# Performance work log

Measured on AMD Instinct MI355X. Metric: run time of the kernel, lower is better.

The kernel has to match this reference:

```python
import jax, jax.numpy as jnp
import numpy as np

N_NODES = 50000
N_EDGES = 800000
IN_FEAT = 256
DIM_H = 64
DIM_OUT = 64


def setup_inputs() -> dict:
    key = jax.random.key(0)
    ks = jax.random.split(key, 9)
    x = jax.random.normal(ks[0], (N_NODES, IN_FEAT), dtype=jnp.float32)
    edge_index = jax.random.randint(ks[1], (2, N_EDGES), 0, N_NODES, dtype=jnp.int64)
    s_in = 1.0 / np.sqrt(IN_FEAT)
    s_h = 1.0 / np.sqrt(DIM_H)
    W_src = jax.random.normal(ks[2], (IN_FEAT, DIM_H), dtype=jnp.float32) * s_in
    W_dst = jax.random.normal(ks[3], (IN_FEAT, DIM_H), dtype=jnp.float32) * s_in
    att_src = jax.random.normal(ks[4], (DIM_H,), dtype=jnp.float32) * s_h
    att_dst = jax.random.normal(ks[5], (DIM_H,), dtype=jnp.float32) * s_h
    bias_conv = jax.random.normal(ks[6], (DIM_H,), dtype=jnp.float32) * 0.01
    W_lin = jax.random.normal(ks[7], (DIM_H, DIM_OUT), dtype=jnp.float32) * s_h
    b_lin = jax.random.normal(ks[8], (DIM_OUT,), dtype=jnp.float32) * 0.01
    return {"x": x, "edge_index": edge_index, "W_src": W_src, "W_dst": W_dst,
            "att_src": att_src, "att_dst": att_dst, "bias_conv": bias_conv,
            "W_lin": W_lin, "b_lin": b_lin}


def reference(x, edge_index, W_src, W_dst, att_src, att_dst, bias_conv, W_lin, b_lin):
    N = x.shape[0]
    src, dst = edge_index[0], edge_index[1]
    # linear projections (GATConv lin_src / lin_dst, no bias)
    h_src = x @ W_src                      # [N, H]
    h_dst = x @ W_dst                      # [N, H]
    # per-node attention logits
    a_src = h_src @ att_src                # [N]
    a_dst = h_dst @ att_dst                # [N]
    # edge-wise score: leaky_relu(a_src[src] + a_dst[dst])
    e = jax.nn.leaky_relu(a_src[src] + a_dst[dst], negative_slope=0.2)  # [E]
    # segment softmax over destination neighborhoods
    e_max = jax.ops.segment_max(e, dst, num_segments=N)
    e_exp = jnp.exp(e - e_max[dst])
    denom = jax.ops.segment_sum(e_exp, dst, num_segments=N)
    alpha = e_exp / denom[dst]             # [E]
    # weighted scatter-add aggregation
    msg = h_src[src] * alpha[:, None]      # [E, H]
    out = jax.ops.segment_sum(msg, dst, num_segments=N) + bias_conv  # [N, H]
    h = jax.nn.relu(out)
    return h @ W_lin + b_lin               # [N, dim_out]
```

## Files before the change

### kernel.cpp

```cpp
#include <hip/hip_runtime.h>
#include <math.h>

#define N_NODES 50000
#define N_EDGES 800000
#define IN_FEAT 256
#define DIM_H   64
#define NPAD    50176
#define CAP     48
#define NBUK    392
#define BNODES  128
#define BCAP    3072
#define EPB     4096
#define PBLKS   784
#define ABLKS   196
#define SPLIT   4
#define PNODES  32

typedef __attribute__((ext_vector_type(8)))  short  s16x8;
typedef __attribute__((ext_vector_type(16))) float  f32x16;

__device__ __forceinline__ float bcast_f(float v, int k) {
  return __int_as_float(__builtin_amdgcn_readlane(__float_as_int(v), k));
}
__device__ __forceinline__ short f2bf(float f) {
  unsigned u = __float_as_uint(f);
  u += 0x7fffu + ((u >> 16) & 1u);
  return (short)(u >> 16);
}

__global__ __launch_bounds__(256, 4) void proj_binA_kernel(
    const float* __restrict__ x,
    const float* __restrict__ Wsrc,
    const float* __restrict__ Wdst,
    const float* __restrict__ att_src,
    const float* __restrict__ att_dst,
    const int* __restrict__ ei,
    unsigned* __restrict__ hbf,
    float* __restrict__ a_src,
    float* __restrict__ a_dst,
    int* __restrict__ gbc,
    unsigned* __restrict__ binbuf) {
  __shared__ short wfrag[16 * 2 * 64 * 8];
  __shared__ float wdl[IN_FEAT];
  __shared__ float attl[DIM_H];

  const int tid = threadIdx.x;

  if (blockIdx.x >= PBLKS) {
    int* bcnt = (int*)wfrag;
    int* wcur = bcnt + NBUK;
    const int e0 = (blockIdx.x - PBLKS) * EPB;

    for (int b = tid; b < NBUK; b += 256) bcnt[b] = 0;
    __syncthreads();

    int dst[16];
    #pragma unroll
    for (int i = 0; i < 16; ++i) {
      int e = e0 + tid + 256 * i;
      dst[i] = (e < N_EDGES) ? ei[N_EDGES + e] : -1;
      if (dst[i] >= 0) atomicAdd(&bcnt[dst[i] >> 7], 1);
    }
    __syncthreads();

    for (int b = tid; b < NBUK; b += 256) {
      int c = bcnt[b];
      wcur[b] = c ? atomicAdd(&gbc[b], c) : 0;
    }
    __syncthreads();

    #pragma unroll
    for (int i = 0; i < 16; ++i) {
      int e = e0 + tid + 256 * i;
      if (e < N_EDGES) {
        int s = ei[e];
        int b = dst[i] >> 7;
        int pos = atomicAdd(&wcur[b], 1);
        if (pos < BCAP)
          binbuf[(long)b * BCAP + pos] =
              (unsigned)s | ((unsigned)(dst[i] & 127) << 16);
      }
    }
    return;
  }

  const int lane = tid & 63;
  const int wv   = tid >> 6;
  const int tile = wv >> 1;
  const int h    = wv & 1;

  if (tid < DIM_H) attl[tid] = att_dst[tid];
  __syncthreads();

  {
    float s = 0.f;
    const float4* row = (const float4*)(Wdst + (long)tid * DIM_H);
    #pragma unroll
    for (int q = 0; q < 16; ++q) {
      float4 r = row[q];
      s = fmaf(r.x, attl[4 * q + 0], s);
      s = fmaf(r.y, attl[4 * q + 1], s);
      s = fmaf(r.z, attl[4 * q + 2], s);
      s = fmaf(r.w, attl[4 * q + 3], s);
    }
    wdl[tid] = s;
  }

  for (int e = tid; e < IN_FEAT * DIM_H; e += 256) {
    int k = e >> 6, n = e & 63;
    int s = k >> 4, half = (k >> 3) & 1, j = k & 7, t = n >> 5;
    int fl = (n & 31) + 32 * half;
    wfrag[((s * 2 + t) * 64 + fl) * 8 + j] = f2bf(Wsrc[e]);
  }
  __syncthreads();

  const int base  = blockIdx.x * 64 + tile * 32;
  int row = base + (lane & 31); if (row > N_NODES - 1) row = N_NODES - 1;
  const int koff8 = (lane >> 5) * 8;
  const int k0    = h * 128;
  const float* px = x + (long)row * IN_FEAT + k0 + koff8;

  f32x16 acc0, acc1;
  #pragma unroll
  for (int i = 0; i < 16; ++i) { acc0[i] = 0.f; acc1[i] = 0.f; }
  float pd = 0.f;

  #pragma unroll
  for (int s = 0; s < 8; ++s) {
    float4 va = *(const float4*)(px + s * 16);
    float4 vb = *(const float4*)(px + s * 16 + 4);
    const float* wp = wdl + k0 + s * 16 + koff8;
    float4 w1 = *(const float4*)(wp);
    float4 w2 = *(const float4*)(wp + 4);
    pd = fmaf(va.x, w1.x, pd); pd = fmaf(va.y, w1.y, pd);
    pd = fmaf(va.z, w1.z, pd); pd = fmaf(va.w, w1.w, pd);
    pd = fmaf(vb.x, w2.x, pd); pd = fmaf(vb.y, w2.y, pd);
    pd = fmaf(vb.z, w2.z, pd); pd = fmaf(vb.w, w2.w, pd);
    s16x8 a;
    a[0] = f2bf(va.x); a[1] = f2bf(va.y); a[2] = f2bf(va.z); a[3] = f2bf(va.w);
    a[4] = f2bf(vb.x); a[5] = f2bf(vb.y); a[6] = f2bf(vb.z); a[7] = f2bf(vb.w);
    const int f = (h * 8 + s) * 2;
    s16x8 b0 = *(const s16x8*)(wfrag + ((f + 0) * 64 + lane) * 8);
    s16x8 b1 = *(const s16x8*)(wfrag + ((f + 1) * 64 + lane) * 8);
    acc0 = __builtin_amdgcn_mfma_f32_32x32x16_bf16(a, b0, acc0, 0, 0, 0);
    acc1 = __builtin_amdgcn_mfma_f32_32x32x16_bf16(a, b1, acc1, 0, 0, 0);
  }
  float pds = pd + __shfl_xor(pd, 32, 64);

  __syncthreads();
  float* fa = (float*)wfrag;
  float* myslot = fa + tile * 2304 + lane * 36;
  float* pdb    = fa + 4608 + tile * 32;

  if (h == 1) {
    #pragma unroll
    for (int i = 0; i < 4; ++i)
      *(float4*)(myslot + i * 4) =
          make_float4(acc0[4 * i], acc0[4 * i + 1], acc0[4 * i + 2], acc0[4 * i + 3]);
    #pragma unroll
    for (int i = 0; i < 4; ++i)
      *(float4*)(myslot + 16 + i * 4) =
          make_float4(acc1[4 * i], acc1[4 * i + 1], acc1[4 * i + 2], acc1[4 * i + 3]);
    if (lane < 32) pdb[lane] = pds;
  }
  __syncthreads();
  if (h == 1) return;

  #pragma unroll
  for (int i = 0; i < 4; ++i) {
    float4 t = *(const float4*)(myslot + i * 4);
    acc0[4 * i] += t.x; acc0[4 * i + 1] += t.y;
    acc0[4 * i + 2] += t.z; acc0[4 * i + 3] += t.w;
  }
  #pragma unroll
  for (int i = 0; i < 4; ++i) {
    float4 t = *(const float4*)(myslot + 16 + i * 4);
    acc1[4 * i] += t.x; acc1[4 * i + 1] += t.y;
    acc1[4 * i + 2] += t.z; acc1[4 * i + 3] += t.w;
  }
  pds += pdb[lane & 31];

  const int col = lane & 31;
  const int rhi = 4 * (lane >> 5);

  #pragma unroll
  for (int r = 0; r < 16; ++r) {
    int node = base + (r & 3) + 8 * (r >> 2) + rhi;
    if (node < N_NODES) {
      unsigned p = (unsigned)(unsigned short)f2bf(acc0[r]) |
                   ((unsigned)(unsigned short)f2bf(acc1[r]) << 16);
      hbf[(long)node * 32 + col] = p;
    }
  }

  float att0 = att_src[col];
  float att1 = att_src[col + 32];
  #pragma unroll
  for (int r = 0; r < 16; ++r) {
    float t = acc0[r] * att0 + acc1[r] * att1;
    t += __shfl_xor(t, 1, 64);
    t += __shfl_xor(t, 2, 64);
    t += __shfl_xor(t, 4, 64);
    t += __shfl_xor(t, 8, 64);
    t += __shfl_xor(t, 16, 64);
    int node = base + (r & 3) + 8 * (r >> 2) + rhi;
    if (col == 0 && node < N_NODES) a_src[node] = t;
  }

  int node = base + (lane & 31);
  if (lane < 32 && node < N_NODES) a_dst[node] = pds;
}

__global__ __launch_bounds__(256) void gatherfused_kernel(
    const unsigned* __restrict__ binbuf,
    const int* __restrict__ gbc,
    const float* __restrict__ a_src,
    const float* __restrict__ a_dst,
    const unsigned* __restrict__ hbf,
    const float* __restrict__ bias_conv,
    const float* __restrict__ W_lin,
    const float* __restrict__ b_lin,
    float* __restrict__ out) {
  __shared__ unsigned rec[PNODES * CAP];
  __shared__ int   lcnt[PNODES];
  __shared__ float adl[PNODES];
  __shared__ float wl[64 * 64];

  const int tid    = threadIdx.x;
  const int bucket = blockIdx.x >> 2;
  const int part   = blockIdx.x & 3;
  const int nb     = bucket * BNODES + part * PNODES;
  const int dlo    = part * PNODES;

  {
    const float4* wsrc4 = (const float4*)W_lin;
    float4* wl4 = (float4*)wl;
    for (int i = tid; i < 1024; i += 256) wl4[i] = wsrc4[i];
  }
  if (tid < PNODES) {
    lcnt[tid] = 0;
    adl[tid]  = a_dst[nb + tid];
  }
  __syncthreads();

  int count = gbc[bucket]; if (count > BCAP) count = BCAP;
  const unsigned* bb = binbuf + (long)bucket * BCAP;
  for (int i = tid; i < count; i += 256) {
    unsigned u = bb[i];
    int dl = (int)(u >> 16) - dlo;
    if ((unsigned)dl < PNODES) {
      int s = (int)(u & 0xffffu);
      float sc = a_src[s] + adl[dl];
      sc = sc >= 0.f ? sc : 0.2f * sc;
      float w = __expf(sc);
      int pos = atomicAdd(&lcnt[dl], 1);
      if (pos < CAP)
        rec[dl * CAP + pos] =
            ((unsigned)(unsigned short)f2bf(w) << 16) | (u & 0xffffu);
    }
  }
  __syncthreads();

  const int lane = tid & 63;
  const int wv   = __builtin_amdgcn_readfirstlane(tid >> 6);
  const int grp8 = lane >> 3;
  const int ql8  = lane & 7;
  const float bj  = bias_conv[lane];
  const float blj = b_lin[lane];

  for (int q = 0; q < 8; ++q) {
    const int dl = wv * 8 + q;
    const int n  = nb + dl;
    int m = lcnt[dl]; if (m > CAP) m = CAP;

    float alo[4] = {0.f, 0.f, 0.f, 0.f};
    float ahi[4] = {0.f, 0.f, 0.f, 0.f};
    float den = 0.f;

    for (int j = 0; j < m; j += 16) {
      int idx0 = j + grp8;
      int idx1 = j + 8 + grp8;
      int ci0 = idx0 < m ? idx0 : m - 1;
      int ci1 = idx1 < m ? idx1 : m - 1;
      unsigned u0 = rec[dl * CAP + ci0];
      unsigned u1 = rec[dl * CAP + ci1];
      float w0 = __uint_as_float(u0 & 0xffff0000u);
      float w1 = __uint_as_float(u1 & 0xffff0000u);
      if (idx0 >= m) w0 = 0.f;
      if (idx1 >= m) w1 = 0.f;
      int s0 = (int)(u0 & 0xffffu);
      int s1 = (int)(u1 & 0xffffu);
      uint4 hp0 = *(const uint4*)(hbf + (long)s0 * 32 + ql8 * 4);
      uint4 hp1 = *(const uint4*)(hbf + (long)s1 * 32 + ql8 * 4);
      alo[0] = fmaf(w0, __uint_as_float(hp0.x << 16),         alo[0]);
      ahi[0] = fmaf(w0, __uint_as_float(hp0.x & 0xffff0000u), ahi[0]);
      alo[1] = fmaf(w0, __uint_as_float(hp0.y << 16),         alo[1]);
      ahi[1] = fmaf(w0, __uint_as_float(hp0.y & 0xffff0000u), ahi[1]);
      alo[2] = fmaf(w0, __uint_as_float(hp0.z << 16),         alo[2]);
      ahi[2] = fmaf(w0, __uint_as_float(hp0.z & 0xffff0000u), ahi[2]);
      alo[3] = fmaf(w0, __uint_as_float(hp0.w << 16),         alo[3]);
      ahi[3] = fmaf(w0, __uint_as_float(hp0.w & 0xffff0000u), ahi[3]);
      den += w0;
      alo[0] = fmaf(w1, __uint_as_float(hp1.x << 16),         alo[0]);
      ahi[0] = fmaf(w1, __uint_as_float(hp1.x & 0xffff0000u), ahi[0]);
      alo[1] = fmaf(w1, __uint_as_float(hp1.y << 16),         alo[1]);
      ahi[1] = fmaf(w1, __uint_as_float(hp1.y & 0xffff0000u), ahi[1]);
      alo[2] = fmaf(w1, __uint_as_float(hp1.z << 16),         alo[2]);
      ahi[2] = fmaf(w1, __uint_as_float(hp1.z & 0xffff0000u), ahi[2]);
      alo[3] = fmaf(w1, __uint_as_float(hp1.w << 16),         alo[3]);
      ahi[3] = fmaf(w1, __uint_as_float(hp1.w & 0xffff0000u), ahi[3]);
      den += w1;
    }

    #pragma unroll
    for (int mm = 8; mm <= 32; mm <<= 1) {
      #pragma unroll
      for (int c = 0; c < 4; ++c) {
        alo[c] += __shfl_xor(alo[c], mm, 64);
        ahi[c] += __shfl_xor(ahi[c], mm, 64);
      }
      den += __shfl_xor(den, mm, 64);
    }
    int srcl = (lane & 31) >> 2;
    float v0 = __shfl(alo[0], srcl, 64);
    float v1 = __shfl(alo[1], srcl, 64);
    float v2 = __shfl(alo[2], srcl, 64);
    float v3 = __shfl(alo[3], srcl, 64);
    float v4 = __shfl(ahi[0], srcl, 64);
    float v5 = __shfl(ahi[1], srcl, 64);
    float v6 = __shfl(ahi[2], srcl, 64);
    float v7 = __shfl(ahi[3], srcl, 64);
    int c4 = lane & 3;
    float losel = (c4 == 0) ? v0 : (c4 == 1) ? v1 : (c4 == 2) ? v2 : v3;
    float hisel = (c4 == 0) ? v4 : (c4 == 1) ? v5 : (c4 == 2) ? v6 : v7;
    float accl = (lane >> 5) ? hisel : losel;

    float inv = den > 0.f ? 1.0f / den : 0.f;
    float z = fmaf(accl, inv, bj);
    float h = fmaxf(z, 0.f);
    float o0 = blj, o1 = 0.f, o2 = 0.f, o3 = 0.f;
    #pragma unroll
    for (int k = 0; k < 64; k += 4) {
      o0 = fmaf(bcast_f(h, k + 0), wl[(k + 0) * 64 + lane], o0);
      o1 = fmaf(bcast_f(h, k + 1), wl[(k + 1) * 64 + lane], o1);
      o2 = fmaf(bcast_f(h, k + 2), wl[(k + 2) * 64 + lane], o2);
      o3 = fmaf(bcast_f(h, k + 3), wl[(k + 3) * 64 + lane], o3);
    }
    float o = (o0 + o1) + (o2 + o3);
    if (n < N_NODES) out[(long)n * DIM_H + lane] = o;
  }
}

extern "C" void kernel_launch(void* const* d_in, const int* in_sizes, int n_in,
                              void* d_out, int out_size, void* d_ws, size_t ws_size,
                              hipStream_t stream) {
  const float* x        = (const float*)d_in[0];
  const int*   ei       = (const int*)d_in[1];
  const float* Wsrc     = (const float*)d_in[2];
  const float* Wdst     = (const float*)d_in[3];
  const float* att_src  = (const float*)d_in[4];
  const float* att_dst  = (const float*)d_in[5];
  const float* bias_cv  = (const float*)d_in[6];
  const float* W_lin    = (const float*)d_in[7];
  const float* b_lin    = (const float*)d_in[8];
  float* out = (float*)d_out;

  unsigned* hbf    = (unsigned*)d_ws;
  float*    a_src  = (float*)(hbf + 1600000);
  float*    a_dst  = a_src + NPAD;
  int*      gbc    = (int*)(a_dst + NPAD);
  unsigned* binbuf = (unsigned*)(gbc + 512);

  hipMemsetAsync(gbc, 0, 512 * sizeof(int), stream);

  proj_binA_kernel<<<PBLKS + ABLKS, 256, 0, stream>>>(
      x, Wsrc, Wdst, att_src, att_dst, ei, hbf, a_src, a_dst, gbc, binbuf);

  gatherfused_kernel<<<NBUK * SPLIT, 256, 0, stream>>>(
      binbuf, gbc, a_src, a_dst, hbf, bias_cv, W_lin, b_lin, out);
}
```

Measured before the change: 176.8 us.

## Bin edges into 32-node buckets so each gather block reads only its edges

The edge binning stage now uses 1568 buckets of 32 destination nodes, where it previously used 392 buckets of 128. Before, each of four gather blocks per bucket scanned all 3072 records and discarded three quarters of them; now each gather block reads exactly its own bucket, which removes that redundant global read and filter work. The W_src bf16 fragment fill is also vectorised to load float4 values. The cost is more global bucket-counter atomics and more shared-memory counters in the binning blocks. Per-bucket capacity (768) has less slack, so it could overflow if degree skew were high.

```diff
diff --git a/kernel.cpp b/kernel.cpp
--- a/kernel.cpp
+++ b/kernel.cpp
@@ -7,13 +7,11 @@
 #define DIM_H   64
 #define NPAD    50176
 #define CAP     48
-#define NBUK    392
-#define BNODES  128
-#define BCAP    3072
+#define NBUK2   1568
+#define BCAP2   768
 #define EPB     4096
 #define PBLKS   784
 #define ABLKS   196
-#define SPLIT   4
 #define PNODES  32
 
 typedef __attribute__((ext_vector_type(8)))  short  s16x8;
@@ -48,10 +46,10 @@
 
   if (blockIdx.x >= PBLKS) {
     int* bcnt = (int*)wfrag;
-    int* wcur = bcnt + NBUK;
+    int* wcur = bcnt + NBUK2;
     const int e0 = (blockIdx.x - PBLKS) * EPB;
 
-    for (int b = tid; b < NBUK; b += 256) bcnt[b] = 0;
+    for (int b = tid; b < NBUK2; b += 256) bcnt[b] = 0;
     __syncthreads();
 
     int dst[16];
@@ -59,11 +57,11 @@
     for (int i = 0; i < 16; ++i) {
       int e = e0 + tid + 256 * i;
       dst[i] = (e < N_EDGES) ? ei[N_EDGES + e] : -1;
-      if (dst[i] >= 0) atomicAdd(&bcnt[dst[i] >> 7], 1);
+      if (dst[i] >= 0) atomicAdd(&bcnt[dst[i] >> 5], 1);
     }
     __syncthreads();
 
-    for (int b = tid; b < NBUK; b += 256) {
+    for (int b = tid; b < NBUK2; b += 256) {
       int c = bcnt[b];
       wcur[b] = c ? atomicAdd(&gbc[b], c) : 0;
     }
@@ -74,11 +72,11 @@
       int e = e0 + tid + 256 * i;
       if (e < N_EDGES) {
         int s = ei[e];
-        int b = dst[i] >> 7;
+        int b = dst[i] >> 5;
         int pos = atomicAdd(&wcur[b], 1);
-        if (pos < BCAP)
-          binbuf[(long)b * BCAP + pos] =
-              (unsigned)s | ((unsigned)(dst[i] & 127) << 16);
+        if (pos < BCAP2)
+          binbuf[(long)b * BCAP2 + pos] =
+              (unsigned)s | ((unsigned)(dst[i] & 31) << 16);
       }
     }
     return;
@@ -106,11 +104,15 @@
     wdl[tid] = s;
   }
 
-  for (int e = tid; e < IN_FEAT * DIM_H; e += 256) {
-    int k = e >> 6, n = e & 63;
-    int s = k >> 4, half = (k >> 3) & 1, j = k & 7, t = n >> 5;
-    int fl = (n & 31) + 32 * half;
-    wfrag[((s * 2 + t) * 64 + fl) * 8 + j] = f2bf(Wsrc[e]);
+  for (int e4 = tid * 4; e4 < IN_FEAT * DIM_H; e4 += 1024) {
+    float4 w4 = *(const float4*)(Wsrc + e4);
+    int k = e4 >> 6, n0 = e4 & 63;
+    int s = k >> 4, half = (k >> 3) & 1, j = k & 7, t = n0 >> 5;
+    short* p = &wfrag[((s * 2 + t) * 64 + ((n0 & 31) + 32 * half)) * 8 + j];
+    p[0]  = f2bf(w4.x);
+    p[8]  = f2bf(w4.y);
+    p[16] = f2bf(w4.z);
+    p[24] = f2bf(w4.w);
   }
   __syncthreads();
 
@@ -227,10 +229,8 @@
   __shared__ float wl[64 * 64];
 
   const int tid    = threadIdx.x;
-  const int bucket = blockIdx.x >> 2;
-  const int part   = blockIdx.x & 3;
-  const int nb     = bucket * BNODES + part * PNODES;
-  const int dlo    = part * PNODES;
+  const int bucket = blockIdx.x;
+  const int nb     = bucket * PNODES;
 
   {
     const float4* wsrc4 = (const float4*)W_lin;
@@ -243,21 +243,19 @@
   }
   __syncthreads();
 
-  int count = gbc[bucket]; if (count > BCAP) count = BCAP;
-  const unsigned* bb = binbuf + (long)bucket * BCAP;
+  int count = gbc[bucket]; if (count > BCAP2) count = BCAP2;
+  const unsigned* bb = binbuf + (long)bucket * BCAP2;
   for (int i = tid; i < count; i += 256) {
     unsigned u = bb[i];
-    int dl = (int)(u >> 16) - dlo;
-    if ((unsigned)dl < PNODES) {
-      int s = (int)(u & 0xffffu);
-      float sc = a_src[s] + adl[dl];
-      sc = sc >= 0.f ? sc : 0.2f * sc;
-      float w = __expf(sc);
-      int pos = atomicAdd(&lcnt[dl], 1);
-      if (pos < CAP)
-        rec[dl * CAP + pos] =
-            ((unsigned)(unsigned short)f2bf(w) << 16) | (u & 0xffffu);
-    }
+    int dl = (int)(u >> 16);
+    int s  = (int)(u & 0xffffu);
+    float sc = a_src[s] + adl[dl];
+    sc = sc >= 0.f ? sc : 0.2f * sc;
+    float w = __expf(sc);
+    int pos = atomicAdd(&lcnt[dl], 1);
+    if (pos < CAP)
+      rec[dl * CAP + pos] =
+          ((unsigned)(unsigned short)f2bf(w) << 16) | (u & 0xffffu);
   }
   __syncthreads();
 
@@ -369,13 +367,13 @@
   float*    a_src  = (float*)(hbf + 1600000);
   float*    a_dst  = a_src + NPAD;
   int*      gbc    = (int*)(a_dst + NPAD);
-  unsigned* binbuf = (unsigned*)(gbc + 512);
-
-  hipMemsetAsync(gbc, 0, 512 * sizeof(int), stream);
+  unsigned* binbuf = (unsigned*)(gbc + 2048);
+
+  hipMemsetAsync(gbc, 0, 2048 * sizeof(int), stream);
 
   proj_binA_kernel<<<PBLKS + ABLKS, 256, 0, stream>>>(
       x, Wsrc, Wdst, att_src, att_dst, ei, hbf, a_src, a_dst, gbc, binbuf);
 
-  gatherfused_kernel<<<NBUK * SPLIT, 256, 0, stream>>>(
+  gatherfused_kernel<<<NBUK2, 256, 0, stream>>>(
       binbuf, gbc, a_src, a_dst, hbf, bias_cv, W_lin, b_lin, out);
 }
```

New measurement: 171.4 us. 3.1% less time.
